# Kernel optimization log

Hardware: AMD Instinct MI355X
Metric: run time of the kernel (lower is better)

## Reference

```python
import jax, jax.numpy as jnp
import numpy as np

HIDDEN_DIM = 512  # H; hidden/encoder feature dim is 2H = 1024


def setup_inputs() -> dict:
    key = jax.random.key(0)
    k1, k2, k3, k4, k5 = jax.random.split(key, 5)
    B, S, D2, H = 16, 4096, 2 * HIDDEN_DIM, HIDDEN_DIM
    hidden = jax.random.normal(k1, (B, D2), dtype=jnp.float32)
    encoder_outputs = jax.random.normal(k2, (B, S, D2), dtype=jnp.float32)
    # nn.Linear(4H, H): weight [H, 4H] in torch; store transposed [4H, H] for x @ W
    W_attn = jax.random.normal(k3, (2 * D2, H), dtype=jnp.float32) * (1.0 / np.sqrt(2 * D2))
    b_attn = jax.random.normal(k4, (H,), dtype=jnp.float32) * 0.01
    # nn.Linear(H, 1, bias=False): weight [1, H] -> vector [H]
    w_v = jax.random.normal(k5, (H,), dtype=jnp.float32) * (1.0 / np.sqrt(H))
    return {"hidden": hidden, "encoder_outputs": encoder_outputs,
            "W_attn": W_attn, "b_attn": b_attn, "w_v": w_v}


def reference(hidden, encoder_outputs, W_attn, b_attn, w_v):
    B, S, D2 = encoder_outputs.shape
    # Broadcast decoder hidden over seq positions and concat with encoder outputs.
    hid = jnp.broadcast_to(hidden[:, None, :], (B, S, D2))
    cat = jnp.concatenate([hid, encoder_outputs], axis=2)        # [B, S, 4H]
    energy = jnp.tanh(cat @ W_attn + b_attn)                      # [B, S, H]
    scores = jnp.einsum('bsh,h->bs', energy, w_v)                 # [B, S]
    attention = jax.nn.softmax(scores, axis=1)                    # [B, S]
    context = jnp.einsum('bs,bsd->bd', attention, encoder_outputs)  # [B, 2H]
    return context
```

## Files before the change

### kernel.cpp

```cpp
#include <hip/hip_runtime.h>
#include <hip/hip_bf16.h>
#include <math.h>

#define HD   512
#define D2   1024
#define SEQ  4096
#define BAT  16
#define BM   128
#define BK   32

typedef _Float16 half8  __attribute__((ext_vector_type(8)));
typedef float    f32x4  __attribute__((ext_vector_type(4)));
typedef float    f32x16 __attribute__((ext_vector_type(16)));

__global__ void wconv_kernel(const float* __restrict__ W, _Float16* __restrict__ WtS) {
  const int kt = blockIdx.x;
  const int nh = blockIdx.y;
  const int t  = threadIdx.x;
  #pragma unroll
  for (int i = 0; i < 4; ++i) {
    const int c   = i * 256 + t;
    const int q   = c >> 9;
    const int kh2 = (c >> 8) & 1;
    const int n   = c & 255;
    half8 h;
    #pragma unroll
    for (int j = 0; j < 8; ++j)
      h[j] = (_Float16)W[(size_t)(D2 + kt * 32 + q * 16 + kh2 * 8 + j) * HD + nh * 256 + n];
    *(half8*)(WtS + ((size_t)(((nh * 32 + kt) * 2 + q) * 2 + kh2) * 256 + n) * 8) = h;
  }
}

__global__ void hproj_kernel(const float* __restrict__ hidden,
                             const float* __restrict__ W,
                             float* __restrict__ hproj) {
  const int b  = blockIdx.x >> 3;
  const int kc = blockIdx.x & 7;
  const int h  = threadIdx.x;
  float a0 = 0.f, a1 = 0.f;
  #pragma unroll 4
  for (int i = 0; i < 128; ++i) {
    const int d = kc * 128 + i;
    const float hd = hidden[b * D2 + d];
    a0 += hd * W[(size_t)d * HD + h];
    a1 += hd * W[(size_t)d * HD + h + 256];
  }
  atomicAdd(&hproj[b * HD + h], a0);
  atomicAdd(&hproj[b * HD + h + 256], a1);
}

__global__ __launch_bounds__(256, 2) void scores_kernel(
    const float* __restrict__ enc, const _Float16* __restrict__ WtS,
    const float* __restrict__ hproj, const float* __restrict__ b_attn,
    const float* __restrict__ w_v, float* __restrict__ scores)
{
  __shared__ __align__(16) _Float16 As[2 * 4 * 128 * 8];

  const int s0   = blockIdx.x * BM;
  const int nh   = blockIdx.y;
  const int b    = blockIdx.z;
  const int tid  = threadIdx.x, lane = tid & 63, w = tid >> 6;
  const int wy   = w >> 1, wx = w & 1;
  const int llo  = lane & 31, lhi = lane >> 5;

  const float* encB = enc + ((size_t)b * SEQ + s0) * D2;

  const int arow = tid >> 1, akc = tid & 1;
  const float* aSrc = encB + (size_t)arow * D2 + akc * 16;

  const _Float16* Bbase = WtS + (size_t)nh * 32 * 8192
                        + lhi * 2048 + wx * 1024 + llo * 8;

  int afOff[2][2];
  #pragma unroll
  for (int mi = 0; mi < 2; ++mi)
    #pragma unroll
    for (int q = 0; q < 2; ++q)
      afOff[mi][q] = ((q * 2 + lhi) * 128 + wy * 64 + mi * 32 + llo) * 8;

  f32x16 acc[2][4];
  #pragma unroll
  for (int mi = 0; mi < 2; ++mi)
    #pragma unroll
    for (int nf = 0; nf < 4; ++nf)
      acc[mi][nf] = (f32x16)(0.f);

  f32x4 R[2][4];

  auto loadA = [&](int kt, f32x4* r) {
    const float* p = aSrc + kt * BK;
    r[0] = *(const f32x4*)(p);
    r[1] = *(const f32x4*)(p + 4);
    r[2] = *(const f32x4*)(p + 8);
    r[3] = *(const f32x4*)(p + 12);
  };
  auto storeA = [&](int buf, const f32x4* r) {
    half8 h0, h1;
    #pragma unroll
    for (int j = 0; j < 4; ++j) {
      h0[j] = (_Float16)r[0][j]; h0[4 + j] = (_Float16)r[1][j];
      h1[j] = (_Float16)r[2][j]; h1[4 + j] = (_Float16)r[3][j];
    }
    *(half8*)&As[((buf * 4 + akc * 2 + 0) * 128 + arow) * 8] = h0;
    *(half8*)&As[((buf * 4 + akc * 2 + 1) * 128 + arow) * 8] = h1;
  };

  loadA(0, R[0]);
  storeA(0, R[0]);
  loadA(1, R[0]);
  loadA(2, R[1]);
  asm volatile("s_waitcnt lgkmcnt(0)\n\ts_barrier" ::: "memory");

  #pragma unroll 2
  for (int kt = 0; kt < 32; ++kt) {
    const int cur = kt & 1, nxt = cur ^ 1;
    const _Float16* Bkt = Bbase + (size_t)kt * 8192;
    half8 bf[2][4];
    #pragma unroll
    for (int q = 0; q < 2; ++q)
      #pragma unroll
      for (int nf = 0; nf < 4; ++nf)
        bf[q][nf] = *(const half8*)(Bkt + q * 4096 + nf * 256);
    half8 af[2][2];
    #pragma unroll
    for (int mi = 0; mi < 2; ++mi)
      #pragma unroll
      for (int q = 0; q < 2; ++q)
        af[mi][q] = *(const half8*)&As[(cur * 4 * 128) * 8 + afOff[mi][q]];
    #pragma unroll
    for (int nf = 0; nf < 4; ++nf)
      #pragma unroll
      for (int mi = 0; mi < 2; ++mi)
        #pragma unroll
        for (int q = 0; q < 2; ++q)
          acc[mi][nf] = __builtin_amdgcn_mfma_f32_32x32x16_f16(af[mi][q], bf[q][nf], acc[mi][nf], 0, 0, 0);
    if (kt + 1 < 32) storeA(nxt, R[kt & 1]);
    if (kt + 3 < 32) loadA(kt + 3, R[kt & 1]);
    asm volatile("s_waitcnt lgkmcnt(0)\n\ts_barrier" ::: "memory");
  }

  float p[2][16];
  #pragma unroll
  for (int mi = 0; mi < 2; ++mi)
    #pragma unroll
    for (int r = 0; r < 16; ++r) p[mi][r] = 0.f;

  #pragma unroll
  for (int nf = 0; nf < 4; ++nf) {
    const int n = nh * 256 + wx * 128 + nf * 32 + llo;
    const float hb = hproj[b * HD + n] + b_attn[n];
    const float wv = w_v[n];
    #pragma unroll
    for (int mi = 0; mi < 2; ++mi)
      #pragma unroll
      for (int r = 0; r < 16; ++r) {
        float x = fminf(fmaxf(acc[mi][nf][r] + hb, -15.f), 15.f);
        float ex = __expf(2.f * x);
        p[mi][r] += wv * __fdividef(ex - 1.f, ex + 1.f);
      }
  }
  #pragma unroll
  for (int off = 1; off <= 16; off <<= 1)
    #pragma unroll
    for (int mi = 0; mi < 2; ++mi)
      #pragma unroll
      for (int r = 0; r < 16; ++r)
        p[mi][r] += __shfl_xor(p[mi][r], off, 64);

  if (llo == 0) {
    #pragma unroll
    for (int mi = 0; mi < 2; ++mi)
      #pragma unroll
      for (int r = 0; r < 16; ++r) {
        const int m = wy * 64 + mi * 32 + (r & 3) + 8 * (r >> 2) + 4 * lhi;
        atomicAdd(&scores[b * SEQ + s0 + m], p[mi][r]);
      }
  }
}

__global__ void softmax_kernel(float* __restrict__ scores) {
  const int b = blockIdx.x;
  float* sc = scores + b * SEQ;
  __shared__ float red[16];
  const int tid = threadIdx.x;
  float loc[16];
  float mx = -1e30f;
  #pragma unroll
  for (int i = 0; i < 16; ++i) { loc[i] = sc[i * 256 + tid]; mx = fmaxf(mx, loc[i]); }
  #pragma unroll
  for (int off = 32; off >= 1; off >>= 1) mx = fmaxf(mx, __shfl_xor(mx, off, 64));
  if ((tid & 63) == 0) red[tid >> 6] = mx;
  __syncthreads();
  mx = fmaxf(fmaxf(red[0], red[1]), fmaxf(red[2], red[3]));
  float sum = 0.f;
  #pragma unroll
  for (int i = 0; i < 16; ++i) { loc[i] = __expf(loc[i] - mx); sum += loc[i]; }
  #pragma unroll
  for (int off = 32; off >= 1; off >>= 1) sum += __shfl_xor(sum, off, 64);
  if ((tid & 63) == 0) red[8 + (tid >> 6)] = sum;
  __syncthreads();
  sum = red[8] + red[9] + red[10] + red[11];
  const float inv = 1.0f / sum;
  #pragma unroll
  for (int i = 0; i < 16; ++i) sc[i * 256 + tid] = loc[i] * inv;
}

__global__ __launch_bounds__(256) void context_kernel(const float* __restrict__ attn,
                                                      const float* __restrict__ enc,
                                                      float* __restrict__ out) {
  const int b  = blockIdx.y;
  const int s0 = blockIdx.x * 64;
  const int tid = threadIdx.x;
  const float* encB = enc + ((size_t)b * SEQ + s0) * D2 + tid * 4;
  const float* at   = attn + b * SEQ + s0;
  f32x4 acc0 = {0.f, 0.f, 0.f, 0.f}, acc1 = {0.f, 0.f, 0.f, 0.f};
  #pragma unroll 8
  for (int i = 0; i < 64; i += 2) {
    acc0 += at[i]     * *(const f32x4*)(encB + (size_t)i * D2);
    acc1 += at[i + 1] * *(const f32x4*)(encB + (size_t)(i + 1) * D2);
  }
  f32x4 acc = acc0 + acc1;
  float* o = out + b * D2 + tid * 4;
  atomicAdd(o + 0, acc[0]);
  atomicAdd(o + 1, acc[1]);
  atomicAdd(o + 2, acc[2]);
  atomicAdd(o + 3, acc[3]);
}

extern "C" void kernel_launch(void* const* d_in, const int* in_sizes, int n_in,
                              void* d_out, int out_size, void* d_ws, size_t ws_size,
                              hipStream_t stream) {
  (void)in_sizes; (void)n_in; (void)ws_size;
  const float* hidden = (const float*)d_in[0];
  const float* enc    = (const float*)d_in[1];
  const float* W      = (const float*)d_in[2];
  const float* b_attn = (const float*)d_in[3];
  const float* w_v    = (const float*)d_in[4];
  float* out = (float*)d_out;

  char* ws = (char*)d_ws;
  _Float16* WtS = (_Float16*)ws;
  float* hproj  = (float*)(ws + (1 << 20));
  float* scores = (float*)(ws + (1 << 20) + 32768);

  hipMemsetAsync(d_out, 0, (size_t)out_size * sizeof(float), stream);
  hipMemsetAsync(hproj, 0, BAT * HD * sizeof(float), stream);
  hipMemsetAsync(scores, 0, (size_t)BAT * SEQ * sizeof(float), stream);

  wconv_kernel  <<<dim3(32, 2),             256, 0, stream>>>(W, WtS);
  hproj_kernel  <<<dim3(128),               256, 0, stream>>>(hidden, W, hproj);
  scores_kernel <<<dim3(SEQ / BM, 2, BAT),  256, 0, stream>>>(enc, WtS, hproj, b_attn, w_v, scores);
  softmax_kernel<<<dim3(BAT),               256, 0, stream>>>(scores);
  context_kernel<<<dim3(SEQ / 64, BAT),     256, 0, stream>>>(scores, enc, out);
}
```

Baseline: 511.9 us.

## Stage B weight tiles through LDS via global_load_lds double buffering

The fp16 weight tiles used as the MFMA B operand are now copied into a double-buffered LDS array with direct global-to-LDS loads, instead of each wave reading them from global memory in registers. The A store and next B issue are moved ahead of the MFMA block, and the hand-written waitcnt+barrier is replaced by __syncthreads. The goal is to cut redundant global/L2 traffic for W and to overlap the B fetch with compute. In exchange it adds 32 KB of LDS per block, which may limit the 2-blocks-per-CU occupancy, and relies on __syncthreads waiting for the global_load_lds vmcnt.

```diff
diff --git a/kernel.cpp b/kernel.cpp
--- a/kernel.cpp
+++ b/kernel.cpp
@@ -12,22 +12,22 @@
 typedef _Float16 half8  __attribute__((ext_vector_type(8)));
 typedef float    f32x4  __attribute__((ext_vector_type(4)));
 typedef float    f32x16 __attribute__((ext_vector_type(16)));
+typedef __attribute__((address_space(3))) void lds_void_t;
+typedef __attribute__((address_space(1))) void glb_void_t;
 
 __global__ void wconv_kernel(const float* __restrict__ W, _Float16* __restrict__ WtS) {
   const int kt = blockIdx.x;
   const int nh = blockIdx.y;
   const int t  = threadIdx.x;
   #pragma unroll
-  for (int i = 0; i < 4; ++i) {
-    const int c   = i * 256 + t;
-    const int q   = c >> 9;
-    const int kh2 = (c >> 8) & 1;
-    const int n   = c & 255;
+  for (int kc = 0; kc < 4; ++kc) {
     half8 h;
     #pragma unroll
-    for (int j = 0; j < 8; ++j)
-      h[j] = (_Float16)W[(size_t)(D2 + kt * 32 + q * 16 + kh2 * 8 + j) * HD + nh * 256 + n];
-    *(half8*)(WtS + ((size_t)(((nh * 32 + kt) * 2 + q) * 2 + kh2) * 256 + n) * 8) = h;
+    for (int j = 0; j < 8; ++j) {
+      const int k = kt * 32 + (kc >> 1) * 16 + (kc & 1) * 8 + j;
+      h[j] = (_Float16)W[(size_t)(D2 + k) * HD + nh * 256 + t];
+    }
+    *(half8*)(WtS + (((size_t)(nh * 32 + kt) * 4 + kc) * 256 + t) * 8) = h;
   }
 }
 
@@ -54,7 +54,8 @@
     const float* __restrict__ hproj, const float* __restrict__ b_attn,
     const float* __restrict__ w_v, float* __restrict__ scores)
 {
-  __shared__ __align__(16) _Float16 As[2 * 4 * 128 * 8];
+  __shared__ __align__(16) _Float16 As[2][4 * 128 * 8];
+  __shared__ __align__(16) _Float16 Bs[2][4 * 256 * 8];
 
   const int s0   = blockIdx.x * BM;
   const int nh   = blockIdx.y;
@@ -65,18 +66,23 @@
 
   const float* encB = enc + ((size_t)b * SEQ + s0) * D2;
 
-  const int arow = tid >> 1, akc = tid & 1;
-  const float* aSrc = encB + (size_t)arow * D2 + akc * 16;
-
-  const _Float16* Bbase = WtS + (size_t)nh * 32 * 8192
-                        + lhi * 2048 + wx * 1024 + llo * 8;
+  const int arow = tid >> 1, akh = tid & 1;
+  const float* aSrc = encB + (size_t)arow * D2 + akh * 16;
+
+  const _Float16* WtB = WtS + (size_t)nh * 32 * 8192;
 
   int afOff[2][2];
   #pragma unroll
   for (int mi = 0; mi < 2; ++mi)
     #pragma unroll
     for (int q = 0; q < 2; ++q)
-      afOff[mi][q] = ((q * 2 + lhi) * 128 + wy * 64 + mi * 32 + llo) * 8;
+      afOff[mi][q] = (((q * 2 + lhi) * 128) + wy * 64 + mi * 32 + llo) * 8;
+  int bfOff[2][4];
+  #pragma unroll
+  for (int q = 0; q < 2; ++q)
+    #pragma unroll
+    for (int nf = 0; nf < 4; ++nf)
+      bfOff[q][nf] = (((q * 2 + lhi) * 256) + wx * 128 + nf * 32 + llo) * 8;
 
   f32x16 acc[2][4];
   #pragma unroll
@@ -101,32 +107,42 @@
       h0[j] = (_Float16)r[0][j]; h0[4 + j] = (_Float16)r[1][j];
       h1[j] = (_Float16)r[2][j]; h1[4 + j] = (_Float16)r[3][j];
     }
-    *(half8*)&As[((buf * 4 + akc * 2 + 0) * 128 + arow) * 8] = h0;
-    *(half8*)&As[((buf * 4 + akc * 2 + 1) * 128 + arow) * 8] = h1;
+    *(half8*)&As[buf][((akh * 2 + 0) * 128 + arow) * 8] = h0;
+    *(half8*)&As[buf][((akh * 2 + 1) * 128 + arow) * 8] = h1;
+  };
+  auto issueB = [&](int kt, int buf) {
+    #pragma unroll
+    for (int i = 0; i < 4; ++i) {
+      const int c = i * 256 + tid;
+      __builtin_amdgcn_global_load_lds(
+          (glb_void_t*)(WtB + ((size_t)kt * 1024 + c) * 8),
+          (lds_void_t*)((char*)&Bs[buf][0] + c * 16), 16, 0, 0);
+    }
   };
 
   loadA(0, R[0]);
   storeA(0, R[0]);
+  issueB(0, 0);
   loadA(1, R[0]);
   loadA(2, R[1]);
-  asm volatile("s_waitcnt lgkmcnt(0)\n\ts_barrier" ::: "memory");
+  __syncthreads();
 
   #pragma unroll 2
   for (int kt = 0; kt < 32; ++kt) {
     const int cur = kt & 1, nxt = cur ^ 1;
-    const _Float16* Bkt = Bbase + (size_t)kt * 8192;
-    half8 bf[2][4];
+    if (kt + 1 < 32) { storeA(nxt, R[cur]); issueB(kt + 1, nxt); }
+    if (kt + 3 < 32) loadA(kt + 3, R[cur]);
+    half8 af[2][2], bf[2][4];
+    #pragma unroll
+    for (int mi = 0; mi < 2; ++mi)
+      #pragma unroll
+      for (int q = 0; q < 2; ++q)
+        af[mi][q] = *(const half8*)&As[cur][afOff[mi][q]];
     #pragma unroll
     for (int q = 0; q < 2; ++q)
       #pragma unroll
       for (int nf = 0; nf < 4; ++nf)
-        bf[q][nf] = *(const half8*)(Bkt + q * 4096 + nf * 256);
-    half8 af[2][2];
-    #pragma unroll
-    for (int mi = 0; mi < 2; ++mi)
-      #pragma unroll
-      for (int q = 0; q < 2; ++q)
-        af[mi][q] = *(const half8*)&As[(cur * 4 * 128) * 8 + afOff[mi][q]];
+        bf[q][nf] = *(const half8*)&Bs[cur][bfOff[q][nf]];
     #pragma unroll
     for (int nf = 0; nf < 4; ++nf)
       #pragma unroll
@@ -134,9 +150,7 @@
         #pragma unroll
         for (int q = 0; q < 2; ++q)
           acc[mi][nf] = __builtin_amdgcn_mfma_f32_32x32x16_f16(af[mi][q], bf[q][nf], acc[mi][nf], 0, 0, 0);
-    if (kt + 1 < 32) storeA(nxt, R[kt & 1]);
-    if (kt + 3 < 32) loadA(kt + 3, R[kt & 1]);
-    asm volatile("s_waitcnt lgkmcnt(0)\n\ts_barrier" ::: "memory");
+    __syncthreads();
   }
 
   float p[2][16];
```

Result: faster. 496.3 us (-3.1%).
